# Kernel optimization log

Measured on AMD Instinct MI355X. Metric: run time of the kernel, lower is better.

## Reference

```python
import jax, jax.numpy as jnp
import numpy as np

BS, S, D_IN, D_EMB = 256, 256, 512, 1024
RATIO = 0.3
BN_EPS = 1e-5
VOCAB = 49408


def setup_inputs() -> dict:
    key = jax.random.key(0)
    ks = jax.random.split(key, 12)
    features = jax.random.normal(ks[0], (BS, S, D_IN), dtype=jnp.float32)
    # variable-length token sequences: nonzero ids up to length, 0-padded
    lengths = jax.random.randint(ks[1], (BS,), 3, S + 1)
    tok = jax.random.randint(ks[2], (BS, S), 1, VOCAB)
    text = jnp.where(jnp.arange(S)[None, :] < lengths[:, None], tok, 0).astype(jnp.int32)
    atten = jax.random.normal(ks[3], (BS, S, S), dtype=jnp.float32)
    sc = 0.02
    H = D_EMB // 2  # 512, MLP hidden
    params = {
        "lin_w": jax.random.normal(ks[4], (D_IN, D_EMB), dtype=jnp.float32) * sc,
        "lin_b": jnp.zeros((D_EMB,), dtype=jnp.float32),
        "w1": jax.random.normal(ks[5], (D_IN, H), dtype=jnp.float32) * sc,
        "b1": jnp.zeros((H,), dtype=jnp.float32),
        "g1": jnp.ones((H,), dtype=jnp.float32),
        "be1": jnp.zeros((H,), dtype=jnp.float32),
        "w2": jax.random.normal(ks[6], (H, D_EMB), dtype=jnp.float32) * sc,
        "b2": jnp.zeros((D_EMB,), dtype=jnp.float32),
        "g2": jnp.ones((D_EMB,), dtype=jnp.float32),
        "be2": jnp.zeros((D_EMB,), dtype=jnp.float32),
    }
    return {"features": features, "text": text, "atten": atten, **params}


def _bn_train(x, g, b):
    # BatchNorm1d in train mode: biased batch stats over rows
    m = x.mean(axis=0)
    v = x.var(axis=0)
    return (x - m) * jax.lax.rsqrt(v + BN_EPS) * g + b


def reference(features, text, atten, lin_w, lin_b, w1, b1, g1, be1, w2, b2, g2, be2):
    bs, seq_len = atten.shape[0], atten.shape[1]
    mask = (text != 0).astype(jnp.float32)          # (bs, S)
    token_lens = mask.sum(axis=1)                   # (bs,)
    k = max(1, int((seq_len - 2) * RATIO))          # static
    eos_pos = jnp.clip(token_lens - 1, 0, seq_len - 1).astype(jnp.int32)
    bidx = jnp.arange(bs)
    # scatter writes into atten (faithful to torch in-place updates)
    atten = atten.at[:, :, 0].set(-1.0)
    atten = atten.at[bidx, :, eos_pos].set(-1.0)
    atten = atten.at[bidx, eos_pos, :].set(-1.0)
    atten_sel = atten[bidx, eos_pos, :] * mask      # (bs, S)
    _, topk_idx = jax.lax.top_k(atten_sel, k)       # (bs, k)
    feats_k = jnp.take_along_axis(features, topk_idx[:, :, None], axis=1)  # (bs,k,D_in)
    norm = jnp.maximum(jnp.linalg.norm(feats_k, axis=-1, keepdims=True), 1e-6)
    feats_k = feats_k / norm
    # linear branch
    cap_emb = jnp.einsum("bkd,de->bke", feats_k, lin_w) + lin_b
    # MLP branch: Linear -> BN -> ReLU -> Linear (last layer no BN/ReLU)
    x = feats_k.reshape(bs * k, -1)
    h = jax.nn.relu(_bn_train(x @ w1 + b1, g1, be1))
    o = (h @ w2 + b2).reshape(bs, k, -1)
    fused = o + cap_emb                             # (bs,k,D_emb)
    # maxk_pool1d_var with k=1: max over first pool_lens[i] positions
    pool_lens = jnp.clip(token_lens - 2, 1, k).astype(jnp.int32)
    valid = jnp.arange(k)[None, :] < pool_lens[:, None]  # (bs,k)
    out = jnp.max(jnp.where(valid[:, :, None], fused, -jnp.inf), axis=1)
    return out.astype(jnp.float32)
```

## Files before the change

### kernel.cpp

```cpp
#include <hip/hip_runtime.h>
#include <hip/hip_bf16.h>

typedef __bf16 bf16;
typedef __bf16 bf16x4 __attribute__((ext_vector_type(4)));
typedef __bf16 bf16x8 __attribute__((ext_vector_type(8)));
typedef float  f32x4  __attribute__((ext_vector_type(4)));

#define BSZ   256
#define SEQ   256
#define DIN   512
#define DEMB  1024
#define KSEL  76
#define MROWS (BSZ * KSEL)
#define MTILES (MROWS / 128)
#define PARTQ (MTILES * 512)
#define NRED  38

__device__ __forceinline__ void gload16(const void* g, void* l) {
  __builtin_amdgcn_global_load_lds((const __attribute__((address_space(1))) void*)g,
                                   (__attribute__((address_space(3))) void*)l, 16, 0, 0);
}

__device__ __forceinline__ unsigned enc(float v) {
  unsigned u = __float_as_uint(v);
  return (u & 0x80000000u) ? ~u : (u | 0x80000000u);
}
__device__ __forceinline__ float dec(unsigned k) {
  return (k & 0x80000000u) ? __uint_as_float(k ^ 0x80000000u) : __uint_as_float(~k);
}

__global__ void k_setup(const int* __restrict__ text, int* __restrict__ topk,
                        int* __restrict__ plen, uint4* __restrict__ keys4,
                        const float* __restrict__ w1, bf16* __restrict__ w1t,
                        const float* __restrict__ lin_w, const float* __restrict__ w2,
                        bf16* __restrict__ b2t,
                        const float* __restrict__ lin_b, const float* __restrict__ b2,
                        float* __restrict__ bias2) {
  int blk = blockIdx.x, tid = threadIdx.x;
  if (blk < 256) {
    int b = blk;
    keys4[b * 256 + tid] = make_uint4(0u, 0u, 0u, 0u);
    __shared__ int red[256];
    red[tid] = (text[b * SEQ + tid] != 0) ? 1 : 0;
    __syncthreads();
    for (int s = 128; s > 0; s >>= 1) {
      if (tid < s) red[tid] += red[tid + s];
      __syncthreads();
    }
    int len = red[0];
    int z = SEQ - len;
    if (tid < KSEL) topk[b * KSEL + tid] = (tid < z) ? (len + tid) : (tid - z);
    if (tid == 0) {
      int p = len - 2;
      plen[b] = p < 1 ? 1 : (p > KSEL ? KSEL : p);
    }
  } else if (blk < 1536) {
    const float* W;
    bf16* Wt;
    int N, ldo, bx, by;
    if (blk < 512)       { int t = blk - 256;  W = w1;    Wt = w1t;       N = 512;  ldo = 512;  bx = t & 15; by = t >> 4; }
    else if (blk < 1024) { int t = blk - 512;  W = lin_w; Wt = b2t;       N = 1024; ldo = 1024; bx = t & 31; by = t >> 5; }
    else                 { int t = blk - 1024; W = w2;    Wt = b2t + 512; N = 1024; ldo = 1024; bx = t & 31; by = t >> 5; }
    __shared__ float tile[32][33];
    int tx = tid & 31, ty = tid >> 5;
    int n = bx * 32 + tx, k0 = by * 32;
#pragma unroll
    for (int r = 0; r < 32; r += 8)
      tile[ty + r][tx] = W[(size_t)(k0 + ty + r) * N + n];
    __syncthreads();
#pragma unroll
    for (int r = 0; r < 32; r += 8)
      Wt[(size_t)(bx * 32 + ty + r) * ldo + k0 + tx] = (bf16)tile[tx][ty + r];
  } else {
    int i = (blk - 1536) * 256 + tid;
    bias2[i] = lin_b[i] + b2[i];
  }
}

__global__ void k_gather(const float* __restrict__ feats, const int* __restrict__ topk,
                         bf16* __restrict__ A2) {
  int r = blockIdx.x;
  int b = r / KSEL;
  int src = topk[r];
  const float4* row = (const float4*)(feats + ((size_t)b * SEQ + src) * DIN);
  int t = threadIdx.x;
  float4 v = row[t];
  float ss = v.x * v.x + v.y * v.y + v.z * v.z + v.w * v.w;
#pragma unroll
  for (int o = 32; o > 0; o >>= 1) ss += __shfl_down(ss, o);
  __shared__ float wsum[2];
  if ((t & 63) == 0) wsum[t >> 6] = ss;
  __syncthreads();
  float total = wsum[0] + wsum[1];
  float inv = 1.0f / fmaxf(sqrtf(total), 1e-6f);
  bf16x4 o4;
  o4.x = (bf16)(v.x * inv);
  o4.y = (bf16)(v.y * inv);
  o4.z = (bf16)(v.z * inv);
  o4.w = (bf16)(v.w * inv);
  ((bf16x4*)A2)[(size_t)r * 256 + t] = o4;
}

template<int EPI>
__global__ __launch_bounds__(256, 2)
void k_gemm(const bf16* __restrict__ A, int lda, const bf16* __restrict__ Bt, int ldb,
            const float* __restrict__ bias, bf16* __restrict__ Cb, int ldc, int Kext,
            float* __restrict__ part, const int* __restrict__ plen,
            unsigned* __restrict__ keys) {
  __shared__ __align__(16) bf16 As[2][128 * 64];
  __shared__ __align__(16) bf16 Bs[2][128 * 64];
  const int m0 = blockIdx.y * 128, n0 = blockIdx.x * 128;
  const int tid = threadIdx.x, w = tid >> 6, lane = tid & 63;
  const int wr = (w >> 1) * 64, wc = (w & 1) * 64;
  const int srow = lane >> 3;
  const int scol = ((lane & 7) ^ srow) * 8;
  const bf16* Ag = A + (size_t)(m0 + w * 32 + srow) * lda + scol;
  const bf16* Bg = Bt + (size_t)(n0 + w * 32 + srow) * ldb + scol;
  const int nT = Kext >> 6;
  f32x4 acc[4][4] = {};
  const int fr = lane & 15, fg = lane >> 4;

  auto stage = [&](int t, int pb) {
    const int kt = t << 6;
#pragma unroll
    for (int c = 0; c < 4; ++c) {
      gload16(Ag + (size_t)(c * 8) * lda + kt, &As[pb][(w * 32 + c * 8) * 64]);
      gload16(Bg + (size_t)(c * 8) * ldb + kt, &Bs[pb][(w * 32 + c * 8) * 64]);
    }
  };

  stage(0, 0);
  for (int t = 0; t < nT; ++t) {
    const int pb = t & 1;
    if (t + 1 < nT) {
      stage(t + 1, pb ^ 1);
      asm volatile("s_waitcnt vmcnt(8)" ::: "memory");
    } else {
      asm volatile("s_waitcnt vmcnt(0)" ::: "memory");
    }
    __builtin_amdgcn_s_barrier();
    __builtin_amdgcn_sched_barrier(0);
#pragma unroll
    for (int kk = 0; kk < 2; ++kk) {
      const int slot = ((kk << 2) | fg) ^ (fr & 7);
      bf16x8 af[4], bfr[4];
#pragma unroll
      for (int i = 0; i < 4; ++i)
        af[i] = *(const bf16x8*)&As[pb][(wr + i * 16 + fr) * 64 + slot * 8];
#pragma unroll
      for (int j = 0; j < 4; ++j)
        bfr[j] = *(const bf16x8*)&Bs[pb][(wc + j * 16 + fr) * 64 + slot * 8];
      __builtin_amdgcn_s_setprio(1);
#pragma unroll
      for (int i = 0; i < 4; ++i)
#pragma unroll
        for (int j = 0; j < 4; ++j)
          acc[i][j] = __builtin_amdgcn_mfma_f32_16x16x32_bf16(af[i], bfr[j], acc[i][j], 0, 0, 0);
      __builtin_amdgcn_s_setprio(0);
    }
    asm volatile("s_waitcnt lgkmcnt(0)" ::: "memory");
    __builtin_amdgcn_s_barrier();
  }

  float bv[4];
#pragma unroll
  for (int j = 0; j < 4; ++j) bv[j] = bias[n0 + wc + j * 16 + fr];

  if (EPI == 1) {
    float s[4] = {0, 0, 0, 0}, q[4] = {0, 0, 0, 0};
#pragma unroll
    for (int i = 0; i < 4; ++i)
#pragma unroll
      for (int v = 0; v < 4; ++v) {
        int r = m0 + wr + i * 16 + fg * 4 + v;
        bf16* crow = Cb + (size_t)r * ldc + n0 + wc + fr;
#pragma unroll
        for (int j = 0; j < 4; ++j) {
          float val = acc[i][j][v] + bv[j];
          crow[j * 16] = (bf16)val;
          s[j] += val;
          q[j] += val * val;
        }
      }
#pragma unroll
    for (int j = 0; j < 4; ++j) {
      s[j] += __shfl_down(s[j], 32); s[j] += __shfl_down(s[j], 16);
      q[j] += __shfl_down(q[j], 32); q[j] += __shfl_down(q[j], 16);
    }
    __syncthreads();
    float* red = (float*)&As[0][0];
    if (lane < 16) {
#pragma unroll
      for (int j = 0; j < 4; ++j) {
        red[(w * 4 + j) * 16 + lane] = s[j];
        red[256 + (w * 4 + j) * 16 + lane] = q[j];
      }
    }
    __syncthreads();
    if (tid < 128) {
      int c = tid;
      int wsel = c >> 6, jj = (c >> 4) & 3, ff = c & 15;
      float ss = red[(wsel * 4 + jj) * 16 + ff] + red[((wsel + 2) * 4 + jj) * 16 + ff];
      float qq = red[256 + (wsel * 4 + jj) * 16 + ff] +
                 red[256 + ((wsel + 2) * 4 + jj) * 16 + ff];
      part[blockIdx.y * 512 + n0 + c] = ss;
      part[PARTQ + blockIdx.y * 512 + n0 + c] = qq;
    }
  } else {
    const float NEG = -__builtin_huge_valf();
    int cur_b = -1, pl = 0;
    bool any = false;
    float cm[4] = {NEG, NEG, NEG, NEG};
#pragma unroll
    for (int i = 0; i < 4; ++i)
#pragma unroll
      for (int v = 0; v < 4; ++v) {
        int gr = m0 + wr + i * 16 + fg * 4 + v;
        int b = gr / KSEL;
        if (b != cur_b) {
          if (any) {
#pragma unroll
            for (int j = 0; j < 4; ++j)
              atomicMax(&keys[(size_t)cur_b * DEMB + n0 + wc + j * 16 + fr], enc(cm[j]));
          }
          cur_b = b;
          pl = plen[b];
          any = false;
#pragma unroll
          for (int j = 0; j < 4; ++j) cm[j] = NEG;
        }
        if (gr - b * KSEL < pl) {
          any = true;
#pragma unroll
          for (int j = 0; j < 4; ++j) cm[j] = fmaxf(cm[j], acc[i][j][v] + bv[j]);
        }
      }
    if (any) {
#pragma unroll
      for (int j = 0; j < 4; ++j)
        atomicMax(&keys[(size_t)cur_b * DEMB + n0 + wc + j * 16 + fr], enc(cm[j]));
    }
  }
}

__global__ void k_bnredA(const float* __restrict__ part, float* __restrict__ part2) {
  int i = blockIdx.x, t = threadIdx.x;
  float s0 = 0, s1 = 0, q0 = 0, q1 = 0;
  for (int j = 0; j < 4; ++j) {
    const float* p = part + (size_t)(i * 4 + j) * 512 + t * 2;
    float2 v = *(const float2*)p;
    float2 u = *(const float2*)(p + PARTQ);
    s0 += v.x; s1 += v.y; q0 += u.x; q1 += u.y;
  }
  part2[i * 512 + t * 2] = s0;
  part2[i * 512 + t * 2 + 1] = s1;
  part2[NRED * 512 + i * 512 + t * 2] = q0;
  part2[NRED * 512 + i * 512 + t * 2 + 1] = q1;
}

__global__ void k_bnstats(const float* __restrict__ part2, const float* __restrict__ g1,
                          const float* __restrict__ be1, float* __restrict__ bns) {
  int c = threadIdx.x;
  float s = 0, q = 0;
  for (int i = 0; i < NRED; ++i) {
    s += part2[i * 512 + c];
    q += part2[NRED * 512 + i * 512 + c];
  }
  const float invn = 1.0f / (float)MROWS;
  float mean = s * invn;
  float var = q * invn - mean * mean;
  float sc = rsqrtf(var + 1e-5f) * g1[c];
  bns[c] = sc;
  bns[512 + c] = be1[c] - mean * sc;
}

__global__ void k_bnapply(bf16x8* __restrict__ A2v, const float* __restrict__ bns) {
  size_t idx = (size_t)blockIdx.x * 256 + threadIdx.x;
  size_t row = idx >> 6;
  int c = (int)(idx & 63);
  bf16x8* p = A2v + row * 128 + 64 + c;
  bf16x8 v = *p;
  int c8 = c * 8;
  const float4 s0 = *(const float4*)(bns + c8);
  const float4 s1 = *(const float4*)(bns + c8 + 4);
  const float4 h0 = *(const float4*)(bns + 512 + c8);
  const float4 h1 = *(const float4*)(bns + 512 + c8 + 4);
  bf16x8 o;
  o[0] = (bf16)fmaxf(fmaf((float)v[0], s0.x, h0.x), 0.0f);
  o[1] = (bf16)fmaxf(fmaf((float)v[1], s0.y, h0.y), 0.0f);
  o[2] = (bf16)fmaxf(fmaf((float)v[2], s0.z, h0.z), 0.0f);
  o[3] = (bf16)fmaxf(fmaf((float)v[3], s0.w, h0.w), 0.0f);
  o[4] = (bf16)fmaxf(fmaf((float)v[4], s1.x, h1.x), 0.0f);
  o[5] = (bf16)fmaxf(fmaf((float)v[5], s1.y, h1.y), 0.0f);
  o[6] = (bf16)fmaxf(fmaf((float)v[6], s1.z, h1.z), 0.0f);
  o[7] = (bf16)fmaxf(fmaf((float)v[7], s1.w, h1.w), 0.0f);
  *p = o;
}

__global__ void k_decode(const unsigned* __restrict__ keys, float* __restrict__ out) {
  int i = blockIdx.x * 256 + threadIdx.x;
  out[i] = dec(keys[i]);
}

extern "C" void kernel_launch(void* const* d_in, const int* in_sizes, int n_in,
                              void* d_out, int out_size, void* d_ws, size_t ws_size,
                              hipStream_t stream) {
  const float* features = (const float*)d_in[0];
  const int*   text     = (const int*)d_in[1];
  const float* lin_w    = (const float*)d_in[3];
  const float* lin_b    = (const float*)d_in[4];
  const float* w1       = (const float*)d_in[5];
  const float* b1       = (const float*)d_in[6];
  const float* g1       = (const float*)d_in[7];
  const float* be1      = (const float*)d_in[8];
  const float* w2       = (const float*)d_in[9];
  const float* b2       = (const float*)d_in[10];
  float* out = (float*)d_out;
  char* ws = (char*)d_ws;

  int*      topk  = (int*)(ws + 0);
  int*      plen  = (int*)(ws + 77824);
  float*    bns   = (float*)(ws + 78848);
  float*    bias2 = (float*)(ws + 82944);
  float*    part  = (float*)(ws + 87040);
  float*    part2 = (float*)(ws + 709632);
  bf16*     w1t   = (bf16*)(ws + 865280);
  bf16*     b2t   = (bf16*)(ws + 1389568);
  bf16*     A2    = (bf16*)(ws + 3486720);
  unsigned* keys  = (unsigned*)(ws + 43332608);

  k_setup<<<1540, 256, 0, stream>>>(text, topk, plen, (uint4*)keys,
                                    w1, w1t, lin_w, w2, b2t, lin_b, b2, bias2);
  k_gather<<<MROWS, 128, 0, stream>>>(features, topk, A2);
  k_gemm<1><<<dim3(4, MTILES), 256, 0, stream>>>(A2, 1024, w1t, 512, b1, A2 + 512, 1024,
                                                 512, part, nullptr, nullptr);
  k_bnredA<<<NRED, 256, 0, stream>>>(part, part2);
  k_bnstats<<<1, 512, 0, stream>>>(part2, g1, be1, bns);
  k_bnapply<<<4864, 256, 0, stream>>>((bf16x8*)A2, bns);
  k_gemm<2><<<dim3(8, MTILES), 256, 0, stream>>>(A2, 1024, b2t, 1024, bias2, nullptr, 0,
                                                 1024, nullptr, plen, keys);
  k_decode<<<BSZ * DEMB / 256, 256, 0, stream>>>(keys, out);
}
```

Baseline: 133.7 us.

## Use 256x128 GEMM tiles with 8 waves, triple-buffered LDS and XCD-aware block remap

Both GEMMs move from 128x128 tiles with 4 waves to 256x128 tiles with 8 waves. Operand loads go into three LDS buffers with a prefetch distance of two, and the A and B stages are interleaved with the two MFMA half-steps. A 1D grid is remapped so that consecutive tiles land on the same XCD, aiming for better L2 reuse. The BN partial reduction is adjusted to the new tile count. The larger LDS footprint (144KB) and 512-thread blocks may reduce occupancy, and the grid remap assumes the block count divides by 8.

```diff
diff --git a/kernel.cpp b/kernel.cpp
--- a/kernel.cpp
+++ b/kernel.cpp
@@ -12,9 +12,9 @@
 #define DEMB  1024
 #define KSEL  76
 #define MROWS (BSZ * KSEL)
-#define MTILES (MROWS / 128)
-#define PARTQ (MTILES * 512)
-#define NRED  38
+#define MT256 (MROWS / 256)
+#define PART76 (MT256 * 512)
+#define NRED  19
 
 __device__ __forceinline__ void gload16(const void* g, void* l) {
   __builtin_amdgcn_global_load_lds((const __attribute__((address_space(1))) void*)g,
@@ -102,109 +102,142 @@
 }
 
 template<int EPI>
-__global__ __launch_bounds__(256, 2)
+__global__ __launch_bounds__(512, 2)
 void k_gemm(const bf16* __restrict__ A, int lda, const bf16* __restrict__ Bt, int ldb,
             const float* __restrict__ bias, bf16* __restrict__ Cb, int ldc, int Kext,
-            float* __restrict__ part, const int* __restrict__ plen,
+            int nbx, float* __restrict__ part, const int* __restrict__ plen,
             unsigned* __restrict__ keys) {
-  __shared__ __align__(16) bf16 As[2][128 * 64];
-  __shared__ __align__(16) bf16 Bs[2][128 * 64];
-  const int m0 = blockIdx.y * 128, n0 = blockIdx.x * 128;
-  const int tid = threadIdx.x, w = tid >> 6, lane = tid & 63;
-  const int wr = (w >> 1) * 64, wc = (w & 1) * 64;
+  __shared__ __align__(16) bf16 As[3][256 * 64];
+  __shared__ __align__(16) bf16 Bs[3][128 * 64];
+  const int q = gridDim.x >> 3;
+  const int lid = blockIdx.x;
+  const int wg = (lid & 7) * q + (lid >> 3);
+  const int bx = wg % nbx, by = wg / nbx;
+  const int m0 = by * 256, n0 = bx * 128;
+  const int tid = threadIdx.x, wid = tid >> 6, lane = tid & 63;
+  const int wm = wid >> 1, wn = wid & 1;
   const int srow = lane >> 3;
   const int scol = ((lane & 7) ^ srow) * 8;
-  const bf16* Ag = A + (size_t)(m0 + w * 32 + srow) * lda + scol;
-  const bf16* Bg = Bt + (size_t)(n0 + w * 32 + srow) * ldb + scol;
+  const bf16* Ag = A + (size_t)(m0 + wid * 16 + srow) * lda + scol;
+  const bf16* Bg = Bt + (size_t)(n0 + wid * 16 + srow) * ldb + scol;
   const int nT = Kext >> 6;
   f32x4 acc[4][4] = {};
   const int fr = lane & 15, fg = lane >> 4;
 
-  auto stage = [&](int t, int pb) {
+  auto stageA = [&](int t, int buf) {
     const int kt = t << 6;
 #pragma unroll
-    for (int c = 0; c < 4; ++c) {
-      gload16(Ag + (size_t)(c * 8) * lda + kt, &As[pb][(w * 32 + c * 8) * 64]);
-      gload16(Bg + (size_t)(c * 8) * ldb + kt, &Bs[pb][(w * 32 + c * 8) * 64]);
+    for (int c = 0; c < 2; ++c) {
+      gload16(Ag + (size_t)(c * 8) * lda + kt, &As[buf][(wid * 16 + c * 8) * 64]);
+      gload16(Ag + (size_t)(128 + c * 8) * lda + kt, &As[buf][(128 + wid * 16 + c * 8) * 64]);
     }
   };
-
-  stage(0, 0);
+  auto stageB = [&](int t, int buf) {
+    const int kt = t << 6;
+#pragma unroll
+    for (int c = 0; c < 2; ++c)
+      gload16(Bg + (size_t)(c * 8) * ldb + kt, &Bs[buf][(wid * 16 + c * 8) * 64]);
+  };
+
+  stageA(0, 0); stageB(0, 0);
+  stageA(1, 1); stageB(1, 1);
+  asm volatile("s_waitcnt vmcnt(6)" ::: "memory");
+  __builtin_amdgcn_s_barrier();
+  __builtin_amdgcn_sched_barrier(0);
+
+  int pb = 0, ps = 2;
   for (int t = 0; t < nT; ++t) {
-    const int pb = t & 1;
-    if (t + 1 < nT) {
-      stage(t + 1, pb ^ 1);
-      asm volatile("s_waitcnt vmcnt(8)" ::: "memory");
+    bf16x8 af[4], bfr[4];
+#pragma unroll
+    for (int i = 0; i < 4; ++i)
+      af[i] = *(const bf16x8*)&As[pb][(wm * 64 + i * 16 + fr) * 64 + (fg ^ (fr & 7)) * 8];
+#pragma unroll
+    for (int j = 0; j < 4; ++j)
+      bfr[j] = *(const bf16x8*)&Bs[pb][(wn * 64 + j * 16 + fr) * 64 + (fg ^ (fr & 7)) * 8];
+    if (t + 2 < nT) stageA(t + 2, ps);
+    __builtin_amdgcn_s_barrier();
+    asm volatile("s_waitcnt lgkmcnt(0)" ::: "memory");
+    __builtin_amdgcn_s_setprio(1);
+#pragma unroll
+    for (int i = 0; i < 4; ++i)
+#pragma unroll
+      for (int j = 0; j < 4; ++j)
+        acc[i][j] = __builtin_amdgcn_mfma_f32_16x16x32_bf16(af[i], bfr[j], acc[i][j], 0, 0, 0);
+    __builtin_amdgcn_s_setprio(0);
+    __builtin_amdgcn_s_barrier();
+#pragma unroll
+    for (int i = 0; i < 4; ++i)
+      af[i] = *(const bf16x8*)&As[pb][(wm * 64 + i * 16 + fr) * 64 + ((4 | fg) ^ (fr & 7)) * 8];
+#pragma unroll
+    for (int j = 0; j < 4; ++j)
+      bfr[j] = *(const bf16x8*)&Bs[pb][(wn * 64 + j * 16 + fr) * 64 + ((4 | fg) ^ (fr & 7)) * 8];
+    if (t + 2 < nT) {
+      stageB(t + 2, ps);
+      asm volatile("s_waitcnt vmcnt(6)" ::: "memory");
     } else {
       asm volatile("s_waitcnt vmcnt(0)" ::: "memory");
     }
     __builtin_amdgcn_s_barrier();
+    asm volatile("s_waitcnt lgkmcnt(0)" ::: "memory");
+    __builtin_amdgcn_s_setprio(1);
+#pragma unroll
+    for (int i = 0; i < 4; ++i)
+#pragma unroll
+      for (int j = 0; j < 4; ++j)
+        acc[i][j] = __builtin_amdgcn_mfma_f32_16x16x32_bf16(af[i], bfr[j], acc[i][j], 0, 0, 0);
+    __builtin_amdgcn_s_setprio(0);
+    __builtin_amdgcn_s_barrier();
     __builtin_amdgcn_sched_barrier(0);
-#pragma unroll
-    for (int kk = 0; kk < 2; ++kk) {
-      const int slot = ((kk << 2) | fg) ^ (fr & 7);
-      bf16x8 af[4], bfr[4];
-#pragma unroll
-      for (int i = 0; i < 4; ++i)
-        af[i] = *(const bf16x8*)&As[pb][(wr + i * 16 + fr) * 64 + slot * 8];
-#pragma unroll
-      for (int j = 0; j < 4; ++j)
-        bfr[j] = *(const bf16x8*)&Bs[pb][(wc + j * 16 + fr) * 64 + slot * 8];
-      __builtin_amdgcn_s_setprio(1);
-#pragma unroll
-      for (int i = 0; i < 4; ++i)
-#pragma unroll
-        for (int j = 0; j < 4; ++j)
-          acc[i][j] = __builtin_amdgcn_mfma_f32_16x16x32_bf16(af[i], bfr[j], acc[i][j], 0, 0, 0);
-      __builtin_amdgcn_s_setprio(0);
-    }
-    asm volatile("s_waitcnt lgkmcnt(0)" ::: "memory");
-    __builtin_amdgcn_s_barrier();
+    pb = (pb == 2) ? 0 : pb + 1;
+    ps = (ps == 2) ? 0 : ps + 1;
   }
 
   float bv[4];
 #pragma unroll
-  for (int j = 0; j < 4; ++j) bv[j] = bias[n0 + wc + j * 16 + fr];
+  for (int j = 0; j < 4; ++j) bv[j] = bias[n0 + wn * 64 + j * 16 + fr];
 
   if (EPI == 1) {
-    float s[4] = {0, 0, 0, 0}, q[4] = {0, 0, 0, 0};
+    float s[4] = {0, 0, 0, 0}, qq_[4] = {0, 0, 0, 0};
 #pragma unroll
     for (int i = 0; i < 4; ++i)
 #pragma unroll
       for (int v = 0; v < 4; ++v) {
-        int r = m0 + wr + i * 16 + fg * 4 + v;
-        bf16* crow = Cb + (size_t)r * ldc + n0 + wc + fr;
+        int r = m0 + wm * 64 + i * 16 + fg * 4 + v;
+        bf16* crow = Cb + (size_t)r * ldc + n0 + wn * 64 + fr;
 #pragma unroll
         for (int j = 0; j < 4; ++j) {
           float val = acc[i][j][v] + bv[j];
           crow[j * 16] = (bf16)val;
           s[j] += val;
-          q[j] += val * val;
+          qq_[j] += val * val;
         }
       }
 #pragma unroll
     for (int j = 0; j < 4; ++j) {
       s[j] += __shfl_down(s[j], 32); s[j] += __shfl_down(s[j], 16);
-      q[j] += __shfl_down(q[j], 32); q[j] += __shfl_down(q[j], 16);
+      qq_[j] += __shfl_down(qq_[j], 32); qq_[j] += __shfl_down(qq_[j], 16);
     }
     __syncthreads();
     float* red = (float*)&As[0][0];
     if (lane < 16) {
 #pragma unroll
       for (int j = 0; j < 4; ++j) {
-        red[(w * 4 + j) * 16 + lane] = s[j];
-        red[256 + (w * 4 + j) * 16 + lane] = q[j];
+        red[(wid * 4 + j) * 16 + lane] = s[j];
+        red[512 + (wid * 4 + j) * 16 + lane] = qq_[j];
       }
     }
     __syncthreads();
     if (tid < 128) {
       int c = tid;
-      int wsel = c >> 6, jj = (c >> 4) & 3, ff = c & 15;
-      float ss = red[(wsel * 4 + jj) * 16 + ff] + red[((wsel + 2) * 4 + jj) * 16 + ff];
-      float qq = red[256 + (wsel * 4 + jj) * 16 + ff] +
-                 red[256 + ((wsel + 2) * 4 + jj) * 16 + ff];
-      part[blockIdx.y * 512 + n0 + c] = ss;
-      part[PARTQ + blockIdx.y * 512 + n0 + c] = qq;
+      int wnsel = c >> 6, jj = (c >> 4) & 3, ff = c & 15;
+      float ss = 0, qs = 0;
+#pragma unroll
+      for (int wmi = 0; wmi < 4; ++wmi) {
+        ss += red[((wmi * 2 + wnsel) * 4 + jj) * 16 + ff];
+        qs += red[512 + ((wmi * 2 + wnsel) * 4 + jj) * 16 + ff];
+      }
+      part[by * 512 + n0 + c] = ss;
+      part[PART76 + by * 512 + n0 + c] = qs;
     }
   } else {
     const float NEG = -__builtin_huge_valf();
@@ -215,13 +248,13 @@
     for (int i = 0; i < 4; ++i)
 #pragma unroll
       for (int v = 0; v < 4; ++v) {
-        int gr = m0 + wr + i * 16 + fg * 4 + v;
+        int gr = m0 + wm * 64 + i * 16 + fg * 4 + v;
         int b = gr / KSEL;
         if (b != cur_b) {
           if (any) {
 #pragma unroll
             for (int j = 0; j < 4; ++j)
-              atomicMax(&keys[(size_t)cur_b * DEMB + n0 + wc + j * 16 + fr], enc(cm[j]));
+              atomicMax(&keys[(size_t)cur_b * DEMB + n0 + wn * 64 + j * 16 + fr], enc(cm[j]));
           }
           cur_b = b;
           pl = plen[b];
@@ -238,7 +271,7 @@
     if (any) {
 #pragma unroll
       for (int j = 0; j < 4; ++j)
-        atomicMax(&keys[(size_t)cur_b * DEMB + n0 + wc + j * 16 + fr], enc(cm[j]));
+        atomicMax(&keys[(size_t)cur_b * DEMB + n0 + wn * 64 + j * 16 + fr], enc(cm[j]));
     }
   }
 }
@@ -249,7 +282,7 @@
   for (int j = 0; j < 4; ++j) {
     const float* p = part + (size_t)(i * 4 + j) * 512 + t * 2;
     float2 v = *(const float2*)p;
-    float2 u = *(const float2*)(p + PARTQ);
+    float2 u = *(const float2*)(p + PART76);
     s0 += v.x; s1 += v.y; q0 += u.x; q1 += u.y;
   }
   part2[i * 512 + t * 2] = s0;
@@ -323,21 +356,21 @@
   float*    bns   = (float*)(ws + 78848);
   float*    bias2 = (float*)(ws + 82944);
   float*    part  = (float*)(ws + 87040);
-  float*    part2 = (float*)(ws + 709632);
-  bf16*     w1t   = (bf16*)(ws + 865280);
-  bf16*     b2t   = (bf16*)(ws + 1389568);
-  bf16*     A2    = (bf16*)(ws + 3486720);
-  unsigned* keys  = (unsigned*)(ws + 43332608);
+  float*    part2 = (float*)(ws + 398336);
+  bf16*     w1t   = (bf16*)(ws + 476160);
+  bf16*     b2t   = (bf16*)(ws + 1000448);
+  bf16*     A2    = (bf16*)(ws + 3097600);
+  unsigned* keys  = (unsigned*)(ws + 42943488);
 
   k_setup<<<1540, 256, 0, stream>>>(text, topk, plen, (uint4*)keys,
                                     w1, w1t, lin_w, w2, b2t, lin_b, b2, bias2);
   k_gather<<<MROWS, 128, 0, stream>>>(features, topk, A2);
-  k_gemm<1><<<dim3(4, MTILES), 256, 0, stream>>>(A2, 1024, w1t, 512, b1, A2 + 512, 1024,
-                                                 512, part, nullptr, nullptr);
+  k_gemm<1><<<MT256 * 4, 512, 0, stream>>>(A2, 1024, w1t, 512, b1, A2 + 512, 1024,
+                                           512, 4, part, nullptr, nullptr);
   k_bnredA<<<NRED, 256, 0, stream>>>(part, part2);
   k_bnstats<<<1, 512, 0, stream>>>(part2, g1, be1, bns);
   k_bnapply<<<4864, 256, 0, stream>>>((bf16x8*)A2, bns);
-  k_gemm<2><<<dim3(8, MTILES), 256, 0, stream>>>(A2, 1024, b2t, 1024, bias2, nullptr, 0,
-                                                 1024, nullptr, plen, keys);
+  k_gemm<2><<<MT256 * 8, 512, 0, stream>>>(A2, 1024, b2t, 1024, bias2, nullptr, 0,
+                                           1024, 8, nullptr, plen, keys);
   k_decode<<<BSZ * DEMB / 256, 256, 0, stream>>>(keys, out);
 }
```

Measured after the change: 125.3 us. -6.3%, faster.

## Deepen GEMM pipeline to four K32 stages with register double-buffering and XCD swizzle

Applied to the files above, without the earlier changes.

The GEMM mainloop moves from a double-buffered K=64 LDS tile to a four-stage ring of K=32 tiles. LDS fragment reads for the next step are issued into a second register set while MFMAs run on the current one. A 1-D grid is remapped so consecutive tiles land on the same XCD, which should improve L2 reuse. The LDS XOR swizzle is dropped, so the 32-wide rows may cause bank conflicts, and the deeper pipeline adds more barriers and waitcnt bookkeeping.

```diff
diff --git a/kernel.cpp b/kernel.cpp
--- a/kernel.cpp
+++ b/kernel.cpp
@@ -12,8 +12,8 @@
 #define DEMB  1024
 #define KSEL  76
 #define MROWS (BSZ * KSEL)
-#define MTILES (MROWS / 128)
-#define PARTQ (MTILES * 512)
+#define MT128 (MROWS / 128)
+#define PARTQ (MT128 * 512)
 #define NRED  38
 
 __device__ __forceinline__ void gload16(const void* g, void* l) {
@@ -101,65 +101,95 @@
   ((bf16x4*)A2)[(size_t)r * 256 + t] = o4;
 }
 
+#define READF(Af, Bf, buf)                                                        \
+  do {                                                                            \
+    _Pragma("unroll")                                                             \
+    for (int i_ = 0; i_ < 4; ++i_)                                                \
+      Af[i_] = *(const bf16x8*)&As[buf][(wr + i_ * 16 + fr) * 32 + fg * 8];       \
+    _Pragma("unroll")                                                             \
+    for (int j_ = 0; j_ < 4; ++j_)                                                \
+      Bf[j_] = *(const bf16x8*)&Bs[buf][(wc + j_ * 16 + fr) * 32 + fg * 8];       \
+  } while (0)
+
+#define MFMA16(Af, Bf)                                                            \
+  do {                                                                            \
+    __builtin_amdgcn_s_setprio(1);                                                \
+    _Pragma("unroll")                                                             \
+    for (int i_ = 0; i_ < 4; ++i_)                                                \
+      _Pragma("unroll")                                                           \
+      for (int j_ = 0; j_ < 4; ++j_)                                              \
+        acc[i_][j_] = __builtin_amdgcn_mfma_f32_16x16x32_bf16(Af[i_], Bf[j_],     \
+                                                              acc[i_][j_], 0, 0, 0); \
+    __builtin_amdgcn_s_setprio(0);                                                \
+  } while (0)
+
 template<int EPI>
 __global__ __launch_bounds__(256, 2)
 void k_gemm(const bf16* __restrict__ A, int lda, const bf16* __restrict__ Bt, int ldb,
             const float* __restrict__ bias, bf16* __restrict__ Cb, int ldc, int Kext,
-            float* __restrict__ part, const int* __restrict__ plen,
+            int nbx, float* __restrict__ part, const int* __restrict__ plen,
             unsigned* __restrict__ keys) {
-  __shared__ __align__(16) bf16 As[2][128 * 64];
-  __shared__ __align__(16) bf16 Bs[2][128 * 64];
-  const int m0 = blockIdx.y * 128, n0 = blockIdx.x * 128;
+  __shared__ __align__(16) bf16 As[4][128 * 32];
+  __shared__ __align__(16) bf16 Bs[4][128 * 32];
+  const int q = gridDim.x >> 3;
+  const int wg = (blockIdx.x & 7) * q + (blockIdx.x >> 3);
+  const int bx = wg % nbx, by = wg / nbx;
+  const int m0 = by * 128, n0 = bx * 128;
   const int tid = threadIdx.x, w = tid >> 6, lane = tid & 63;
   const int wr = (w >> 1) * 64, wc = (w & 1) * 64;
-  const int srow = lane >> 3;
-  const int scol = ((lane & 7) ^ srow) * 8;
-  const bf16* Ag = A + (size_t)(m0 + w * 32 + srow) * lda + scol;
-  const bf16* Bg = Bt + (size_t)(n0 + w * 32 + srow) * ldb + scol;
-  const int nT = Kext >> 6;
+  const int srow = lane >> 2, scol = (lane & 3) * 8;
+  const bf16* Ag0 = A + (size_t)(m0 + w * 16 + srow) * lda + scol;
+  const bf16* Ag1 = Ag0 + (size_t)64 * lda;
+  const bf16* Bg0 = Bt + (size_t)(n0 + w * 16 + srow) * ldb + scol;
+  const bf16* Bg1 = Bg0 + (size_t)64 * ldb;
+  const int nT = Kext >> 5;
   f32x4 acc[4][4] = {};
   const int fr = lane & 15, fg = lane >> 4;
 
-  auto stage = [&](int t, int pb) {
-    const int kt = t << 6;
-#pragma unroll
-    for (int c = 0; c < 4; ++c) {
-      gload16(Ag + (size_t)(c * 8) * lda + kt, &As[pb][(w * 32 + c * 8) * 64]);
-      gload16(Bg + (size_t)(c * 8) * ldb + kt, &Bs[pb][(w * 32 + c * 8) * 64]);
-    }
+  auto stage = [&](int t, int buf) {
+    const int kt = t << 5;
+    gload16(Ag0 + kt, &As[buf][(w * 16) * 32]);
+    gload16(Ag1 + kt, &As[buf][(w * 16 + 64) * 32]);
+    gload16(Bg0 + kt, &Bs[buf][(w * 16) * 32]);
+    gload16(Bg1 + kt, &Bs[buf][(w * 16 + 64) * 32]);
   };
 
-  stage(0, 0);
-  for (int t = 0; t < nT; ++t) {
-    const int pb = t & 1;
-    if (t + 1 < nT) {
-      stage(t + 1, pb ^ 1);
-      asm volatile("s_waitcnt vmcnt(8)" ::: "memory");
-    } else {
-      asm volatile("s_waitcnt vmcnt(0)" ::: "memory");
-    }
+  bf16x8 A0[4], B0[4], A1[4], B1[4];
+
+  stage(0, 0); stage(1, 1); stage(2, 2);
+  asm volatile("s_waitcnt vmcnt(8)" ::: "memory");
+  __builtin_amdgcn_s_barrier();
+  __builtin_amdgcn_sched_barrier(0);
+  READF(A0, B0, 0);
+  stage(3, 3);
+  asm volatile("s_waitcnt lgkmcnt(0)" ::: "memory");
+  asm volatile("s_waitcnt vmcnt(8)" ::: "memory");
+  __builtin_amdgcn_s_barrier();
+  __builtin_amdgcn_sched_barrier(0);
+
+  for (int t = 0; t < nT; t += 2) {
+    if (t + 4 < nT) stage(t + 4, (t + 4) & 3);
+    READF(A1, B1, (t + 1) & 3);
+    __builtin_amdgcn_sched_barrier(0);
+    MFMA16(A0, B0);
+    asm volatile("s_waitcnt lgkmcnt(0)" ::: "memory");
+    __builtin_amdgcn_sched_barrier(0);
+    if (t + 4 < nT)       asm volatile("s_waitcnt vmcnt(8)" ::: "memory");
+    else if (t + 3 < nT)  asm volatile("s_waitcnt vmcnt(4)" ::: "memory");
+    else                  asm volatile("s_waitcnt vmcnt(0)" ::: "memory");
     __builtin_amdgcn_s_barrier();
     __builtin_amdgcn_sched_barrier(0);
-#pragma unroll
-    for (int kk = 0; kk < 2; ++kk) {
-      const int slot = ((kk << 2) | fg) ^ (fr & 7);
-      bf16x8 af[4], bfr[4];
-#pragma unroll
-      for (int i = 0; i < 4; ++i)
-        af[i] = *(const bf16x8*)&As[pb][(wr + i * 16 + fr) * 64 + slot * 8];
-#pragma unroll
-      for (int j = 0; j < 4; ++j)
-        bfr[j] = *(const bf16x8*)&Bs[pb][(wc + j * 16 + fr) * 64 + slot * 8];
-      __builtin_amdgcn_s_setprio(1);
-#pragma unroll
-      for (int i = 0; i < 4; ++i)
-#pragma unroll
-        for (int j = 0; j < 4; ++j)
-          acc[i][j] = __builtin_amdgcn_mfma_f32_16x16x32_bf16(af[i], bfr[j], acc[i][j], 0, 0, 0);
-      __builtin_amdgcn_s_setprio(0);
-    }
+    if (t + 5 < nT) stage(t + 5, (t + 5) & 3);
+    if (t + 2 < nT) READF(A0, B0, (t + 2) & 3);
+    __builtin_amdgcn_sched_barrier(0);
+    MFMA16(A1, B1);
     asm volatile("s_waitcnt lgkmcnt(0)" ::: "memory");
+    __builtin_amdgcn_sched_barrier(0);
+    if (t + 5 < nT)       asm volatile("s_waitcnt vmcnt(8)" ::: "memory");
+    else if (t + 4 < nT)  asm volatile("s_waitcnt vmcnt(4)" ::: "memory");
+    else                  asm volatile("s_waitcnt vmcnt(0)" ::: "memory");
     __builtin_amdgcn_s_barrier();
+    __builtin_amdgcn_sched_barrier(0);
   }
 
   float bv[4];
@@ -167,7 +197,7 @@
   for (int j = 0; j < 4; ++j) bv[j] = bias[n0 + wc + j * 16 + fr];
 
   if (EPI == 1) {
-    float s[4] = {0, 0, 0, 0}, q[4] = {0, 0, 0, 0};
+    float s[4] = {0, 0, 0, 0}, qq_[4] = {0, 0, 0, 0};
 #pragma unroll
     for (int i = 0; i < 4; ++i)
 #pragma unroll
@@ -179,13 +209,13 @@
           float val = acc[i][j][v] + bv[j];
           crow[j * 16] = (bf16)val;
           s[j] += val;
-          q[j] += val * val;
+          qq_[j] += val * val;
         }
       }
 #pragma unroll
     for (int j = 0; j < 4; ++j) {
       s[j] += __shfl_down(s[j], 32); s[j] += __shfl_down(s[j], 16);
-      q[j] += __shfl_down(q[j], 32); q[j] += __shfl_down(q[j], 16);
+      qq_[j] += __shfl_down(qq_[j], 32); qq_[j] += __shfl_down(qq_[j], 16);
     }
     __syncthreads();
     float* red = (float*)&As[0][0];
@@ -193,7 +223,7 @@
 #pragma unroll
       for (int j = 0; j < 4; ++j) {
         red[(w * 4 + j) * 16 + lane] = s[j];
-        red[256 + (w * 4 + j) * 16 + lane] = q[j];
+        red[256 + (w * 4 + j) * 16 + lane] = qq_[j];
       }
     }
     __syncthreads();
@@ -201,10 +231,10 @@
       int c = tid;
       int wsel = c >> 6, jj = (c >> 4) & 3, ff = c & 15;
       float ss = red[(wsel * 4 + jj) * 16 + ff] + red[((wsel + 2) * 4 + jj) * 16 + ff];
-      float qq = red[256 + (wsel * 4 + jj) * 16 + ff] +
+      float qs = red[256 + (wsel * 4 + jj) * 16 + ff] +
                  red[256 + ((wsel + 2) * 4 + jj) * 16 + ff];
-      part[blockIdx.y * 512 + n0 + c] = ss;
-      part[PARTQ + blockIdx.y * 512 + n0 + c] = qq;
+      part[by * 512 + n0 + c] = ss;
+      part[PARTQ + by * 512 + n0 + c] = qs;
     }
   } else {
     const float NEG = -__builtin_huge_valf();
@@ -332,12 +362,12 @@
   k_setup<<<1540, 256, 0, stream>>>(text, topk, plen, (uint4*)keys,
                                     w1, w1t, lin_w, w2, b2t, lin_b, b2, bias2);
   k_gather<<<MROWS, 128, 0, stream>>>(features, topk, A2);
-  k_gemm<1><<<dim3(4, MTILES), 256, 0, stream>>>(A2, 1024, w1t, 512, b1, A2 + 512, 1024,
-                                                 512, part, nullptr, nullptr);
+  k_gemm<1><<<MT128 * 4, 256, 0, stream>>>(A2, 1024, w1t, 512, b1, A2 + 512, 1024,
+                                           512, 4, part, nullptr, nullptr);
   k_bnredA<<<NRED, 256, 0, stream>>>(part, part2);
   k_bnstats<<<1, 512, 0, stream>>>(part2, g1, be1, bns);
   k_bnapply<<<4864, 256, 0, stream>>>((bf16x8*)A2, bns);
-  k_gemm<2><<<dim3(8, MTILES), 256, 0, stream>>>(A2, 1024, b2t, 1024, bias2, nullptr, 0,
-                                                 1024, nullptr, plen, keys);
+  k_gemm<2><<<MT128 * 8, 256, 0, stream>>>(A2, 1024, b2t, 1024, bias2, nullptr, 0,
+                                           1024, 8, nullptr, plen, keys);
   k_decode<<<BSZ * DEMB / 256, 256, 0, stream>>>(keys, out);
 }
```

New measurement: 143.9 us. 1.08x slower.

## Single-buffer GEMM LDS, raise occupancy, and remap blocks across XCDs

Applied to the files above, without the earlier changes.

Replaces the double-buffered LDS pipeline in the GEMM with a single buffer synchronised by two __syncthreads per K step. This halves LDS use so launch bounds can rise to 4 blocks per CU, relying on other resident blocks to hide global load latency instead of in-block prefetch. It also moves to a 1D grid whose block index is permuted in groups of 8, so consecutive tiles land on the same XCD for better L2 locality. The cost is that load/compute overlap within a block is lost, the setprio hints are dropped, and register pressure is tighter under the higher occupancy bound.

```diff
diff --git a/kernel.cpp b/kernel.cpp
--- a/kernel.cpp
+++ b/kernel.cpp
@@ -12,8 +12,8 @@
 #define DEMB  1024
 #define KSEL  76
 #define MROWS (BSZ * KSEL)
-#define MTILES (MROWS / 128)
-#define PARTQ (MTILES * 512)
+#define MT128 (MROWS / 128)
+#define PARTQ (MT128 * 512)
 #define NRED  38
 
 __device__ __forceinline__ void gload16(const void* g, void* l) {
@@ -102,64 +102,50 @@
 }
 
 template<int EPI>
-__global__ __launch_bounds__(256, 2)
+__global__ __launch_bounds__(256, 4)
 void k_gemm(const bf16* __restrict__ A, int lda, const bf16* __restrict__ Bt, int ldb,
             const float* __restrict__ bias, bf16* __restrict__ Cb, int ldc, int Kext,
-            float* __restrict__ part, const int* __restrict__ plen,
+            int nbx, float* __restrict__ part, const int* __restrict__ plen,
             unsigned* __restrict__ keys) {
-  __shared__ __align__(16) bf16 As[2][128 * 64];
-  __shared__ __align__(16) bf16 Bs[2][128 * 64];
-  const int m0 = blockIdx.y * 128, n0 = blockIdx.x * 128;
+  __shared__ __align__(16) bf16 As[128 * 64];
+  __shared__ __align__(16) bf16 Bs[128 * 64];
+  const int q = gridDim.x >> 3;
+  const int wg = (blockIdx.x & 7) * q + (blockIdx.x >> 3);
+  const int bx = wg % nbx, by = wg / nbx;
+  const int m0 = by * 128, n0 = bx * 128;
   const int tid = threadIdx.x, w = tid >> 6, lane = tid & 63;
   const int wr = (w >> 1) * 64, wc = (w & 1) * 64;
   const int srow = lane >> 3;
   const int scol = ((lane & 7) ^ srow) * 8;
   const bf16* Ag = A + (size_t)(m0 + w * 32 + srow) * lda + scol;
   const bf16* Bg = Bt + (size_t)(n0 + w * 32 + srow) * ldb + scol;
-  const int nT = Kext >> 6;
   f32x4 acc[4][4] = {};
   const int fr = lane & 15, fg = lane >> 4;
 
-  auto stage = [&](int t, int pb) {
-    const int kt = t << 6;
+  for (int kt = 0; kt < Kext; kt += 64) {
+    __syncthreads();
 #pragma unroll
     for (int c = 0; c < 4; ++c) {
-      gload16(Ag + (size_t)(c * 8) * lda + kt, &As[pb][(w * 32 + c * 8) * 64]);
-      gload16(Bg + (size_t)(c * 8) * ldb + kt, &Bs[pb][(w * 32 + c * 8) * 64]);
-    }
-  };
-
-  stage(0, 0);
-  for (int t = 0; t < nT; ++t) {
-    const int pb = t & 1;
-    if (t + 1 < nT) {
-      stage(t + 1, pb ^ 1);
-      asm volatile("s_waitcnt vmcnt(8)" ::: "memory");
-    } else {
-      asm volatile("s_waitcnt vmcnt(0)" ::: "memory");
-    }
-    __builtin_amdgcn_s_barrier();
-    __builtin_amdgcn_sched_barrier(0);
+      gload16(Ag + (size_t)(c * 8) * lda + kt, &As[(w * 32 + c * 8) * 64]);
+      gload16(Bg + (size_t)(c * 8) * ldb + kt, &Bs[(w * 32 + c * 8) * 64]);
+    }
+    __syncthreads();
 #pragma unroll
     for (int kk = 0; kk < 2; ++kk) {
       const int slot = ((kk << 2) | fg) ^ (fr & 7);
       bf16x8 af[4], bfr[4];
 #pragma unroll
       for (int i = 0; i < 4; ++i)
-        af[i] = *(const bf16x8*)&As[pb][(wr + i * 16 + fr) * 64 + slot * 8];
+        af[i] = *(const bf16x8*)&As[(wr + i * 16 + fr) * 64 + slot * 8];
 #pragma unroll
       for (int j = 0; j < 4; ++j)
-        bfr[j] = *(const bf16x8*)&Bs[pb][(wc + j * 16 + fr) * 64 + slot * 8];
-      __builtin_amdgcn_s_setprio(1);
+        bfr[j] = *(const bf16x8*)&Bs[(wc + j * 16 + fr) * 64 + slot * 8];
 #pragma unroll
       for (int i = 0; i < 4; ++i)
 #pragma unroll
         for (int j = 0; j < 4; ++j)
           acc[i][j] = __builtin_amdgcn_mfma_f32_16x16x32_bf16(af[i], bfr[j], acc[i][j], 0, 0, 0);
-      __builtin_amdgcn_s_setprio(0);
-    }
-    asm volatile("s_waitcnt lgkmcnt(0)" ::: "memory");
-    __builtin_amdgcn_s_barrier();
+    }
   }
 
   float bv[4];
@@ -167,7 +153,7 @@
   for (int j = 0; j < 4; ++j) bv[j] = bias[n0 + wc + j * 16 + fr];
 
   if (EPI == 1) {
-    float s[4] = {0, 0, 0, 0}, q[4] = {0, 0, 0, 0};
+    float s[4] = {0, 0, 0, 0}, qq_[4] = {0, 0, 0, 0};
 #pragma unroll
     for (int i = 0; i < 4; ++i)
 #pragma unroll
@@ -179,21 +165,21 @@
           float val = acc[i][j][v] + bv[j];
           crow[j * 16] = (bf16)val;
           s[j] += val;
-          q[j] += val * val;
+          qq_[j] += val * val;
         }
       }
 #pragma unroll
     for (int j = 0; j < 4; ++j) {
       s[j] += __shfl_down(s[j], 32); s[j] += __shfl_down(s[j], 16);
-      q[j] += __shfl_down(q[j], 32); q[j] += __shfl_down(q[j], 16);
-    }
-    __syncthreads();
-    float* red = (float*)&As[0][0];
+      qq_[j] += __shfl_down(qq_[j], 32); qq_[j] += __shfl_down(qq_[j], 16);
+    }
+    __syncthreads();
+    float* red = (float*)&As[0];
     if (lane < 16) {
 #pragma unroll
       for (int j = 0; j < 4; ++j) {
         red[(w * 4 + j) * 16 + lane] = s[j];
-        red[256 + (w * 4 + j) * 16 + lane] = q[j];
+        red[256 + (w * 4 + j) * 16 + lane] = qq_[j];
       }
     }
     __syncthreads();
@@ -201,10 +187,10 @@
       int c = tid;
       int wsel = c >> 6, jj = (c >> 4) & 3, ff = c & 15;
       float ss = red[(wsel * 4 + jj) * 16 + ff] + red[((wsel + 2) * 4 + jj) * 16 + ff];
-      float qq = red[256 + (wsel * 4 + jj) * 16 + ff] +
+      float qs = red[256 + (wsel * 4 + jj) * 16 + ff] +
                  red[256 + ((wsel + 2) * 4 + jj) * 16 + ff];
-      part[blockIdx.y * 512 + n0 + c] = ss;
-      part[PARTQ + blockIdx.y * 512 + n0 + c] = qq;
+      part[by * 512 + n0 + c] = ss;
+      part[PARTQ + by * 512 + n0 + c] = qs;
     }
   } else {
     const float NEG = -__builtin_huge_valf();
@@ -332,12 +318,12 @@
   k_setup<<<1540, 256, 0, stream>>>(text, topk, plen, (uint4*)keys,
                                     w1, w1t, lin_w, w2, b2t, lin_b, b2, bias2);
   k_gather<<<MROWS, 128, 0, stream>>>(features, topk, A2);
-  k_gemm<1><<<dim3(4, MTILES), 256, 0, stream>>>(A2, 1024, w1t, 512, b1, A2 + 512, 1024,
-                                                 512, part, nullptr, nullptr);
+  k_gemm<1><<<MT128 * 4, 256, 0, stream>>>(A2, 1024, w1t, 512, b1, A2 + 512, 1024,
+                                           512, 4, part, nullptr, nullptr);
   k_bnredA<<<NRED, 256, 0, stream>>>(part, part2);
   k_bnstats<<<1, 512, 0, stream>>>(part2, g1, be1, bns);
   k_bnapply<<<4864, 256, 0, stream>>>((bf16x8*)A2, bns);
-  k_gemm<2><<<dim3(8, MTILES), 256, 0, stream>>>(A2, 1024, b2t, 1024, bias2, nullptr, 0,
-                                                 1024, nullptr, plen, keys);
+  k_gemm<2><<<MT128 * 8, 256, 0, stream>>>(A2, 1024, b2t, 1024, bias2, nullptr, 0,
+                                           1024, 8, nullptr, plen, keys);
   k_decode<<<BSZ * DEMB / 256, 256, 0, stream>>>(keys, out);
 }
```

After: 110.2 us (median of 2 runs). 17.6% less time.
